# Kernel optimization log

Hardware: AMD Instinct MI355X
Metric: run time of the kernel (lower is better)

## Reference

```python
import jax, jax.numpy as jnp
import numpy as np

N_NODES = 50000


def gcn_conv(x, edge_index, W, b):
    """PyG GCNConv: add self-loops, sym-normalize, out = A_hat @ (x W) + b."""
    src, dst = edge_index[0], edge_index[1]
    n = x.shape[0]
    h = x @ W  # [N, out]
    # degree with self-loops (all edge weights = 1)
    deg = jax.ops.segment_sum(jnp.ones_like(dst, dtype=x.dtype), dst, num_segments=n) + 1.0
    dinv = jax.lax.rsqrt(deg)  # deg >= 1 so safe
    norm = dinv[src] * dinv[dst]  # [E]
    msgs = h[src] * norm[:, None]  # gather + scale
    agg = jax.ops.segment_sum(msgs, dst, num_segments=n)  # scatter-add
    agg = agg + h * (dinv * dinv)[:, None]  # self-loop term: norm_ii = dinv_i^2
    return agg + b


def setup_inputs() -> dict:
    key = jax.random.key(0)
    k_x, k_e, k_w1, k_w2 = jax.random.split(key, 4)
    in_ch, hid, out_ch = 256, 128, 128
    x = jax.random.normal(k_x, (N_NODES, in_ch), dtype=jnp.float32)
    edge_index = jax.random.randint(k_e, (2, 1_600_000), 0, N_NODES, dtype=jnp.int32)
    # Glorot-style init like PyG GCNConv
    W1 = jax.random.normal(k_w1, (in_ch, hid), dtype=jnp.float32) * (1.0 / np.sqrt(in_ch))
    b1 = jnp.zeros((hid,), dtype=jnp.float32)
    W2 = jax.random.normal(k_w2, (hid, out_ch), dtype=jnp.float32) * (1.0 / np.sqrt(hid))
    b2 = jnp.zeros((out_ch,), dtype=jnp.float32)
    return {"x": x, "edge_index": edge_index, "W1": W1, "b1": b1, "W2": W2, "b2": b2}


def reference(x, edge_index, W1, b1, W2, b2):
    # layer 1: GCNConv -> ReLU (dropout is identity in eval mode)
    h = jax.nn.relu(gcn_conv(x, edge_index, W1, b1))
    # layer 2: GCNConv -> ReLU
    out = jax.nn.relu(gcn_conv(h, edge_index, W2, b2))
    return out
```

## Files before the change

### kernel.cpp

```cpp
#include <hip/hip_runtime.h>
#include <cstdint>
#include <cstddef>


#define ELL_STRIDE 64
#define BCAP 8192
#define OVF_CAP 1024
#define PART_T 2048

typedef __attribute__((ext_vector_type(8))) short bf16x8;
typedef __attribute__((ext_vector_type(4))) float floatx4;

__device__ __forceinline__ unsigned short f2bf(float f) {
  unsigned int u = __float_as_uint(f);
  unsigned int r = (u + 0x7fffu + ((u >> 16) & 1u)) >> 16;
  return (unsigned short)r;
}
__device__ __forceinline__ float2 bfpair(unsigned int p) {
  float2 r;
  r.x = __uint_as_float(p << 16);
  r.y = __uint_as_float(p & 0xffff0000u);
  return r;
}

__global__ __launch_bounds__(256) void k_cvt_w(const float* __restrict__ W1,
                                               const float* __restrict__ W2,
                                               unsigned short* __restrict__ WT1,
                                               unsigned short* __restrict__ WT2,
                                               int* __restrict__ cursor,
                                               int* __restrict__ ovf_cnt,
                                               int NB) {
  int i = blockIdx.x * 256 + threadIdx.x;
  if (i < NB) cursor[i] = 0;
  if (i == NB) *ovf_cnt = 0;
  if (i < 128 * 256) {
    int n = i >> 8, k = i & 255;
    WT1[i] = f2bf(W1[k * 128 + n]);
  } else if (i < 128 * 256 + 128 * 128) {
    int j = i - 128 * 256;
    int n = j >> 7, k = j & 127;
    WT2[j] = f2bf(W2[k * 128 + n]);
  }
}

__global__ __launch_bounds__(256) void k_part(const int* __restrict__ src,
                                              const int* __restrict__ dst,
                                              int* __restrict__ cursor,
                                              unsigned int* __restrict__ part,
                                              int* __restrict__ ovf_cnt,
                                              int* __restrict__ ovf,
                                              int E, int NB) {
  __shared__ unsigned int stage1[PART_T];
  __shared__ unsigned int stage2[PART_T];
  __shared__ int hist[512];
  __shared__ int base_g[512];
  __shared__ int base_l[512];
  __shared__ int cl[512];
  __shared__ int sc[256];
  const int tid = threadIdx.x;
  const int e0 = blockIdx.x * PART_T;
  int valid = E - e0; if (valid > PART_T) valid = PART_T;

  hist[tid] = 0; hist[tid + 256] = 0;
  cl[tid] = 0; cl[tid + 256] = 0;
  __syncthreads();
  for (int i = tid; i < valid; i += 256) {
    int e = e0 + i;
    unsigned int v = (unsigned int)(src[e] & 0xffff) | ((unsigned int)dst[e] << 16);
    stage1[i] = v;
    atomicAdd(&hist[(v >> 16) >> 7], 1);
  }
  __syncthreads();
  for (int b = tid; b < NB; b += 256) base_g[b] = atomicAdd(&cursor[b], hist[b]);
  int h0 = hist[2 * tid], h1 = hist[2 * tid + 1];
  int pv = h0 + h1;
  sc[tid] = pv;
  __syncthreads();
  #pragma unroll
  for (int off = 1; off < 256; off <<= 1) {
    int t = (tid >= off) ? sc[tid - off] : 0;
    __syncthreads();
    sc[tid] += t;
    __syncthreads();
  }
  int excl = sc[tid] - pv;
  base_l[2 * tid] = excl;
  base_l[2 * tid + 1] = excl + h0;
  __syncthreads();
  for (int i = tid; i < valid; i += 256) {
    unsigned int v = stage1[i];
    int b = (v >> 16) >> 7;
    int pos = base_l[b] + atomicAdd(&cl[b], 1);
    stage2[pos] = v;
  }
  __syncthreads();
  for (int i = tid; i < valid; i += 256) {
    unsigned int v = stage2[i];
    int b = (v >> 16) >> 7;
    int g = base_g[b] + (i - base_l[b]);
    if (g < BCAP) {
      part[(size_t)b * BCAP + g] = v;
    } else {
      int p = atomicAdd(ovf_cnt, 1);
      if (p < OVF_CAP) { ovf[2 * p] = (int)(v & 0xffffu); ovf[2 * p + 1] = (int)(v >> 16); }
    }
  }
}

__global__ __launch_bounds__(256) void k_fill2(const unsigned int* __restrict__ part,
                                               const int* __restrict__ cursor,
                                               unsigned short* __restrict__ col,
                                               int* __restrict__ cnt,
                                               float* __restrict__ dinv,
                                               int* __restrict__ ovf_cnt,
                                               int* __restrict__ ovf, int N) {
  __shared__ unsigned short slab[128 * ELL_STRIDE];
  __shared__ int cl[128];
  const int tid = threadIdx.x;
  const int b = blockIdx.x;
  if (tid < 128) cl[tid] = 0;
  __syncthreads();
  int count = cursor[b]; if (count > BCAP) count = BCAP;
  const unsigned int* p = part + (size_t)b * BCAP;
  for (int i = tid; i < count; i += 256) {
    unsigned int v = p[i];
    int row = (v >> 16) & 127;
    int k = atomicAdd(&cl[row], 1);
    if (k < ELL_STRIDE) {
      slab[row * ELL_STRIDE + k] = (unsigned short)(v & 0xffffu);
    } else {
      int q = atomicAdd(ovf_cnt, 1);
      if (q < OVF_CAP) { ovf[2 * q] = (int)(v & 0xffffu); ovf[2 * q + 1] = (int)(v >> 16); }
    }
  }
  __syncthreads();
  uint4* d4 = (uint4*)(col + (size_t)b * 128 * ELL_STRIDE);
  const uint4* s4 = (const uint4*)slab;
  #pragma unroll
  for (int i = 0; i < (128 * ELL_STRIDE * 2) / (16 * 256); ++i)
    d4[i * 256 + tid] = s4[i * 256 + tid];
  if (tid < 128) {
    int node = b * 128 + tid;
    if (node < N) {
      int c = cl[tid];
      cnt[node] = c;
      dinv[node] = rsqrtf((float)c + 1.0f);
    }
  }
}

template <int K, bool AF32>
__global__ __launch_bounds__(256) void k_gemm_mfma(const void* __restrict__ Xv,
                                                   const unsigned short* __restrict__ WT,
                                                   const float* __restrict__ dinv,
                                                   unsigned short* __restrict__ hb,
                                                   int M) {
  constexpr int KP = K + 8;
  __shared__ unsigned short Bs[64 * KP];
  const int tid = threadIdx.x;
  const int wave = tid >> 6, lane = tid & 63;
  const int q = lane >> 4, m = lane & 15;
  const int row0 = blockIdx.x * 64 + wave * 16;
  const bool active = row0 < M;
  const int arow = row0 + m;

  floatx4 acc[8];
  #pragma unroll
  for (int nt = 0; nt < 8; ++nt) acc[nt] = (floatx4){0.f, 0.f, 0.f, 0.f};
  bf16x8 af[K / 32];

  #pragma unroll
  for (int half = 0; half < 2; ++half) {
    __syncthreads();
    for (int c = tid; c < 64 * (K / 8); c += 256) {
      int r = c / (K / 8), ko = (c % (K / 8)) * 8;
      *(uint4*)(Bs + r * KP + ko) =
          *(const uint4*)(WT + (size_t)(half * 64 + r) * K + ko);
    }
    __syncthreads();
    if (active) {
      #pragma unroll
      for (int ks = 0; ks < K / 32; ++ks) {
        const int k0 = ks * 32 + q * 8;
        if (half == 0) {
          if (AF32) {
            const float* X = (const float*)Xv;
            float4 a0 = *(const float4*)(X + (size_t)arow * K + k0);
            float4 a1 = *(const float4*)(X + (size_t)arow * K + k0 + 4);
            af[ks] = (bf16x8){(short)f2bf(a0.x), (short)f2bf(a0.y),
                              (short)f2bf(a0.z), (short)f2bf(a0.w),
                              (short)f2bf(a1.x), (short)f2bf(a1.y),
                              (short)f2bf(a1.z), (short)f2bf(a1.w)};
          } else {
            af[ks] = *(const bf16x8*)((const unsigned short*)Xv +
                                      (size_t)arow * K + k0);
          }
        }
        #pragma unroll
        for (int ntl = 0; ntl < 4; ++ntl) {
          bf16x8 bf = *(const bf16x8*)(Bs + (ntl * 16 + m) * KP + k0);
          acc[half * 4 + ntl] =
              __builtin_amdgcn_mfma_f32_16x16x32_bf16(af[ks], bf, acc[half * 4 + ntl],
                                                      0, 0, 0);
        }
      }
    }
  }
  if (!active) return;
  #pragma unroll
  for (int r = 0; r < 4; ++r) {
    int grow = row0 + q * 4 + r;
    float di = dinv[grow];
    #pragma unroll
    for (int nt = 0; nt < 8; ++nt)
      hb[(size_t)(nt >> 1) * M * 32 + (size_t)grow * 32 + (nt & 1) * 16 + m] =
          f2bf(acc[nt][r] * di);
  }
}

template <bool BF16OUT>
__global__ __launch_bounds__(256) void k_agg(const unsigned int* __restrict__ hb,
                                             const int* __restrict__ cnt,
                                             const unsigned short* __restrict__ col,
                                             const float* __restrict__ dinv,
                                             const int* __restrict__ ovf_cnt,
                                             const int* __restrict__ ovf,
                                             const float* __restrict__ bias,
                                             void* __restrict__ outv, int n) {
  const int tid = threadIdx.x;
  const int chunk = blockIdx.x & 3;
  const int nb = blockIdx.x >> 2;
  const int d = nb * 16 + (tid >> 4);
  const int u = tid & 15;
  if (d >= n) return;
  const unsigned int* slab = hb + (size_t)chunk * n * 16;

  float2 acc = bfpair(slab[(size_t)d * 16 + u]);

  int m = cnt[d]; if (m > ELL_STRIDE) m = ELL_STRIDE;
  const unsigned short* crow = col + (size_t)d * ELL_STRIDE;
  int k = 0;
  for (; k + 8 <= m; k += 8) {
    ushort4 ca = *(const ushort4*)(crow + k);
    ushort4 cb = *(const ushort4*)(crow + k + 4);
    unsigned int p0 = slab[(size_t)ca.x * 16 + u];
    unsigned int p1 = slab[(size_t)ca.y * 16 + u];
    unsigned int p2 = slab[(size_t)ca.z * 16 + u];
    unsigned int p3 = slab[(size_t)ca.w * 16 + u];
    unsigned int p4 = slab[(size_t)cb.x * 16 + u];
    unsigned int p5 = slab[(size_t)cb.y * 16 + u];
    unsigned int p6 = slab[(size_t)cb.z * 16 + u];
    unsigned int p7 = slab[(size_t)cb.w * 16 + u];
    float2 v0 = bfpair(p0), v1 = bfpair(p1), v2 = bfpair(p2), v3 = bfpair(p3);
    float2 v4 = bfpair(p4), v5 = bfpair(p5), v6 = bfpair(p6), v7 = bfpair(p7);
    acc.x += v0.x + v1.x + v2.x + v3.x + v4.x + v5.x + v6.x + v7.x;
    acc.y += v0.y + v1.y + v2.y + v3.y + v4.y + v5.y + v6.y + v7.y;
  }
  for (; k < m; ++k) {
    int c = crow[k];
    float2 v = bfpair(slab[(size_t)c * 16 + u]);
    acc.x += v.x; acc.y += v.y;
  }
  int V = *ovf_cnt; if (V > OVF_CAP) V = OVF_CAP;
  for (int j = 0; j < V; ++j) {
    if (ovf[2 * j + 1] == d) {
      float2 v = bfpair(slab[(size_t)ovf[2 * j] * 16 + u]);
      acc.x += v.x; acc.y += v.y;
    }
  }
  float di = dinv[d];
  float2 bv = *(const float2*)(bias + chunk * 32 + 2 * u);
  float rx = fmaxf(di * acc.x + bv.x, 0.f);
  float ry = fmaxf(di * acc.y + bv.y, 0.f);
  if (BF16OUT) {
    unsigned int pk = (unsigned int)f2bf(rx) | ((unsigned int)f2bf(ry) << 16);
    ((unsigned int*)outv)[(size_t)d * 64 + chunk * 16 + u] = pk;
  } else {
    *(float2*)((float*)outv + (size_t)d * 128 + chunk * 32 + 2 * u) =
        make_float2(rx, ry);
  }
}

extern "C" void kernel_launch(void* const* d_in, const int* in_sizes, int n_in,
                              void* d_out, int out_size, void* d_ws, size_t ws_size,
                              hipStream_t stream) {
  const float* x  = (const float*)d_in[0];
  const int*   ei = (const int*)d_in[1];
  const float* W1 = (const float*)d_in[2];
  const float* b1 = (const float*)d_in[3];
  const float* W2 = (const float*)d_in[4];
  const float* b2 = (const float*)d_in[5];
  float* out = (float*)d_out;

  const int IN_CH = 256;
  const int N = in_sizes[0] / IN_CH;
  const int E = in_sizes[1] / 2;
  const int NB = (N + 127) >> 7;

  const int* src = ei;
  const int* dst = ei + E;

  char* ws = (char*)d_ws;
  size_t off = 0;
  auto carve = [&](size_t bytes) {
    void* p = ws + off;
    off += (bytes + 255) & ~(size_t)255;
    return p;
  };
  int*            cursor  = (int*)carve((size_t)NB * 4);
  int*            ovf_cnt = (int*)carve(4);
  int*            ovf     = (int*)carve((size_t)OVF_CAP * 2 * 4);
  int*            cnt     = (int*)carve((size_t)N * 4);
  float*          dinv    = (float*)carve((size_t)N * 4);
  unsigned short* col     = (unsigned short*)carve((size_t)N * ELL_STRIDE * 2);
  unsigned short* hb      = (unsigned short*)carve((size_t)N * 128 * 2);
  unsigned short* WT1     = (unsigned short*)carve(128 * 256 * 2);
  unsigned short* WT2     = (unsigned short*)carve(128 * 128 * 2);
  char*           unionp  = (char*)carve((size_t)NB * BCAP * 4);
  unsigned int*   part    = (unsigned int*)unionp;
  unsigned short* aggbuf  = (unsigned short*)unionp;

  k_cvt_w<<<(128 * 256 + 128 * 128 + 255) / 256, 256, 0, stream>>>(
      W1, W2, WT1, WT2, cursor, ovf_cnt, NB);
  k_part <<<(E + PART_T - 1) / PART_T, 256, 0, stream>>>(src, dst, cursor, part,
                                                         ovf_cnt, ovf, E, NB);
  k_fill2<<<NB, 256, 0, stream>>>(part, cursor, col, cnt, dinv, ovf_cnt, ovf, N);

  int gblocks = (N + 63) / 64;
  int ablocks = 4 * ((N + 15) / 16);
  k_gemm_mfma<256, true ><<<gblocks, 256, 0, stream>>>(x, WT1, dinv, hb, N);
  k_agg<true ><<<ablocks, 256, 0, stream>>>((const unsigned int*)hb, cnt, col, dinv,
                                            ovf_cnt, ovf, b1, aggbuf, N);
  k_gemm_mfma<128, false><<<gblocks, 256, 0, stream>>>(aggbuf, WT2, dinv, hb, N);
  k_agg<false><<<ablocks, 256, 0, stream>>>((const unsigned int*)hb, cnt, col, dinv,
                                            ovf_cnt, ovf, b2, out, N);
}
```

Baseline: 266.5 us.

## Load full weight tile once in GEMM and widen aggregation gathers

The GEMM kernel now uses 512-thread blocks that stage the whole transposed weight matrix in shared memory once, instead of in two halves with extra barriers, and issues all 8 MFMA column tiles per k-step. The aggregation kernel stages each block's 32 ELL column lists in shared memory, gives each node 8 lanes that load 8-byte bf16 quads instead of 16 lanes loading 4-byte pairs, and unrolls the gather loop to 16 neighbours. The aim is fewer global index loads and more memory-level parallelism per thread. The cost is higher LDS use per GEMM block and more registers in the aggregation kernel, which could lower occupancy.

```diff
diff --git a/kernel.cpp b/kernel.cpp
--- a/kernel.cpp
+++ b/kernel.cpp
@@ -150,63 +150,59 @@
 }
 
 template <int K, bool AF32>
-__global__ __launch_bounds__(256) void k_gemm_mfma(const void* __restrict__ Xv,
+__global__ __launch_bounds__(512) void k_gemm_mfma(const void* __restrict__ Xv,
                                                    const unsigned short* __restrict__ WT,
                                                    const float* __restrict__ dinv,
                                                    unsigned short* __restrict__ hb,
                                                    int M) {
   constexpr int KP = K + 8;
-  __shared__ unsigned short Bs[64 * KP];
+  __shared__ unsigned short Bs[128 * KP];
   const int tid = threadIdx.x;
   const int wave = tid >> 6, lane = tid & 63;
   const int q = lane >> 4, m = lane & 15;
-  const int row0 = blockIdx.x * 64 + wave * 16;
+  const int row0 = blockIdx.x * 128 + wave * 16;
   const bool active = row0 < M;
   const int arow = row0 + m;
 
+  for (int c = tid; c < 128 * (K / 8); c += 512) {
+    int r = c / (K / 8), ko = (c % (K / 8)) * 8;
+    *(uint4*)(Bs + r * KP + ko) = *(const uint4*)(WT + (size_t)r * K + ko);
+  }
+
+  bf16x8 af[K / 32];
+  if (active) {
+    #pragma unroll
+    for (int ks = 0; ks < K / 32; ++ks) {
+      const int k0 = ks * 32 + q * 8;
+      if (AF32) {
+        const float* X = (const float*)Xv;
+        float4 a0 = *(const float4*)(X + (size_t)arow * K + k0);
+        float4 a1 = *(const float4*)(X + (size_t)arow * K + k0 + 4);
+        af[ks] = (bf16x8){(short)f2bf(a0.x), (short)f2bf(a0.y),
+                          (short)f2bf(a0.z), (short)f2bf(a0.w),
+                          (short)f2bf(a1.x), (short)f2bf(a1.y),
+                          (short)f2bf(a1.z), (short)f2bf(a1.w)};
+      } else {
+        af[ks] = *(const bf16x8*)((const unsigned short*)Xv +
+                                  (size_t)arow * K + k0);
+      }
+    }
+  }
+  __syncthreads();
+  if (!active) return;
+
   floatx4 acc[8];
   #pragma unroll
   for (int nt = 0; nt < 8; ++nt) acc[nt] = (floatx4){0.f, 0.f, 0.f, 0.f};
-  bf16x8 af[K / 32];
-
-  #pragma unroll
-  for (int half = 0; half < 2; ++half) {
-    __syncthreads();
-    for (int c = tid; c < 64 * (K / 8); c += 256) {
-      int r = c / (K / 8), ko = (c % (K / 8)) * 8;
-      *(uint4*)(Bs + r * KP + ko) =
-          *(const uint4*)(WT + (size_t)(half * 64 + r) * K + ko);
-    }
-    __syncthreads();
-    if (active) {
-      #pragma unroll
-      for (int ks = 0; ks < K / 32; ++ks) {
-        const int k0 = ks * 32 + q * 8;
-        if (half == 0) {
-          if (AF32) {
-            const float* X = (const float*)Xv;
-            float4 a0 = *(const float4*)(X + (size_t)arow * K + k0);
-            float4 a1 = *(const float4*)(X + (size_t)arow * K + k0 + 4);
-            af[ks] = (bf16x8){(short)f2bf(a0.x), (short)f2bf(a0.y),
-                              (short)f2bf(a0.z), (short)f2bf(a0.w),
-                              (short)f2bf(a1.x), (short)f2bf(a1.y),
-                              (short)f2bf(a1.z), (short)f2bf(a1.w)};
-          } else {
-            af[ks] = *(const bf16x8*)((const unsigned short*)Xv +
-                                      (size_t)arow * K + k0);
-          }
-        }
-        #pragma unroll
-        for (int ntl = 0; ntl < 4; ++ntl) {
-          bf16x8 bf = *(const bf16x8*)(Bs + (ntl * 16 + m) * KP + k0);
-          acc[half * 4 + ntl] =
-              __builtin_amdgcn_mfma_f32_16x16x32_bf16(af[ks], bf, acc[half * 4 + ntl],
-                                                      0, 0, 0);
-        }
-      }
-    }
-  }
-  if (!active) return;
+  #pragma unroll
+  for (int ks = 0; ks < K / 32; ++ks) {
+    const int k0 = ks * 32 + q * 8;
+    #pragma unroll
+    for (int nt = 0; nt < 8; ++nt) {
+      bf16x8 bf = *(const bf16x8*)(Bs + (nt * 16 + m) * KP + k0);
+      acc[nt] = __builtin_amdgcn_mfma_f32_16x16x32_bf16(af[ks], bf, acc[nt], 0, 0, 0);
+    }
+  }
   #pragma unroll
   for (int r = 0; r < 4; ++r) {
     int grow = row0 + q * 4 + r;
@@ -227,57 +223,103 @@
                                              const int* __restrict__ ovf,
                                              const float* __restrict__ bias,
                                              void* __restrict__ outv, int n) {
+  __shared__ unsigned short cols[32][ELL_STRIDE];
   const int tid = threadIdx.x;
   const int chunk = blockIdx.x & 3;
-  const int nb = blockIdx.x >> 2;
-  const int d = nb * 16 + (tid >> 4);
-  const int u = tid & 15;
+  const int nd0 = (blockIdx.x >> 2) * 32;
+  {
+    int s = tid * 16;
+    int node = nd0 + (s >> 6);
+    uint4 v0 = make_uint4(0, 0, 0, 0), v1 = v0;
+    if (node < n) {
+      v0 = *(const uint4*)(col + (size_t)node * ELL_STRIDE + (s & 63));
+      v1 = *(const uint4*)(col + (size_t)node * ELL_STRIDE + (s & 63) + 8);
+    }
+    *(uint4*)&cols[s >> 6][s & 63] = v0;
+    *(uint4*)&cols[s >> 6][(s & 63) + 8] = v1;
+  }
+  __syncthreads();
+  const int nodeL = tid >> 3;
+  const int d = nd0 + nodeL;
+  const int w = tid & 7;
   if (d >= n) return;
-  const unsigned int* slab = hb + (size_t)chunk * n * 16;
-
-  float2 acc = bfpair(slab[(size_t)d * 16 + u]);
+  const uint2* slab = (const uint2*)hb + (size_t)chunk * n * 8;
+  const unsigned short* lc = cols[nodeL];
+
+  uint2 sv = slab[(size_t)d * 8 + w];
+  float2 s0 = bfpair(sv.x), s1 = bfpair(sv.y);
+  float a0 = s0.x, a1 = s0.y, a2 = s1.x, a3 = s1.y;
 
   int m = cnt[d]; if (m > ELL_STRIDE) m = ELL_STRIDE;
-  const unsigned short* crow = col + (size_t)d * ELL_STRIDE;
   int k = 0;
+#define GATH(P)                                                   \
+  {                                                               \
+    float2 _x = bfpair((P).x), _y = bfpair((P).y);                \
+    a0 += _x.x; a1 += _x.y; a2 += _y.x; a3 += _y.y;               \
+  }
+  for (; k + 16 <= m; k += 16) {
+    ushort4 ca = *(const ushort4*)(lc + k);
+    ushort4 cb = *(const ushort4*)(lc + k + 4);
+    ushort4 cc = *(const ushort4*)(lc + k + 8);
+    ushort4 cd = *(const ushort4*)(lc + k + 12);
+    uint2 p0 = slab[(size_t)ca.x * 8 + w];
+    uint2 p1 = slab[(size_t)ca.y * 8 + w];
+    uint2 p2 = slab[(size_t)ca.z * 8 + w];
+    uint2 p3 = slab[(size_t)ca.w * 8 + w];
+    uint2 p4 = slab[(size_t)cb.x * 8 + w];
+    uint2 p5 = slab[(size_t)cb.y * 8 + w];
+    uint2 p6 = slab[(size_t)cb.z * 8 + w];
+    uint2 p7 = slab[(size_t)cb.w * 8 + w];
+    uint2 p8 = slab[(size_t)cc.x * 8 + w];
+    uint2 p9 = slab[(size_t)cc.y * 8 + w];
+    uint2 pa = slab[(size_t)cc.z * 8 + w];
+    uint2 pb = slab[(size_t)cc.w * 8 + w];
+    uint2 pc = slab[(size_t)cd.x * 8 + w];
+    uint2 pd = slab[(size_t)cd.y * 8 + w];
+    uint2 pe = slab[(size_t)cd.z * 8 + w];
+    uint2 pf = slab[(size_t)cd.w * 8 + w];
+    GATH(p0) GATH(p1) GATH(p2) GATH(p3) GATH(p4) GATH(p5) GATH(p6) GATH(p7)
+    GATH(p8) GATH(p9) GATH(pa) GATH(pb) GATH(pc) GATH(pd) GATH(pe) GATH(pf)
+  }
   for (; k + 8 <= m; k += 8) {
-    ushort4 ca = *(const ushort4*)(crow + k);
-    ushort4 cb = *(const ushort4*)(crow + k + 4);
-    unsigned int p0 = slab[(size_t)ca.x * 16 + u];
-    unsigned int p1 = slab[(size_t)ca.y * 16 + u];
-    unsigned int p2 = slab[(size_t)ca.z * 16 + u];
-    unsigned int p3 = slab[(size_t)ca.w * 16 + u];
-    unsigned int p4 = slab[(size_t)cb.x * 16 + u];
-    unsigned int p5 = slab[(size_t)cb.y * 16 + u];
-    unsigned int p6 = slab[(size_t)cb.z * 16 + u];
-    unsigned int p7 = slab[(size_t)cb.w * 16 + u];
-    float2 v0 = bfpair(p0), v1 = bfpair(p1), v2 = bfpair(p2), v3 = bfpair(p3);
-    float2 v4 = bfpair(p4), v5 = bfpair(p5), v6 = bfpair(p6), v7 = bfpair(p7);
-    acc.x += v0.x + v1.x + v2.x + v3.x + v4.x + v5.x + v6.x + v7.x;
-    acc.y += v0.y + v1.y + v2.y + v3.y + v4.y + v5.y + v6.y + v7.y;
+    ushort4 ca = *(const ushort4*)(lc + k);
+    ushort4 cb = *(const ushort4*)(lc + k + 4);
+    uint2 p0 = slab[(size_t)ca.x * 8 + w];
+    uint2 p1 = slab[(size_t)ca.y * 8 + w];
+    uint2 p2 = slab[(size_t)ca.z * 8 + w];
+    uint2 p3 = slab[(size_t)ca.w * 8 + w];
+    uint2 p4 = slab[(size_t)cb.x * 8 + w];
+    uint2 p5 = slab[(size_t)cb.y * 8 + w];
+    uint2 p6 = slab[(size_t)cb.z * 8 + w];
+    uint2 p7 = slab[(size_t)cb.w * 8 + w];
+    GATH(p0) GATH(p1) GATH(p2) GATH(p3) GATH(p4) GATH(p5) GATH(p6) GATH(p7)
   }
   for (; k < m; ++k) {
-    int c = crow[k];
-    float2 v = bfpair(slab[(size_t)c * 16 + u]);
-    acc.x += v.x; acc.y += v.y;
+    uint2 p = slab[(size_t)lc[k] * 8 + w];
+    GATH(p)
   }
   int V = *ovf_cnt; if (V > OVF_CAP) V = OVF_CAP;
   for (int j = 0; j < V; ++j) {
     if (ovf[2 * j + 1] == d) {
-      float2 v = bfpair(slab[(size_t)ovf[2 * j] * 16 + u]);
-      acc.x += v.x; acc.y += v.y;
-    }
-  }
+      uint2 p = slab[(size_t)ovf[2 * j] * 8 + w];
+      GATH(p)
+    }
+  }
+#undef GATH
   float di = dinv[d];
-  float2 bv = *(const float2*)(bias + chunk * 32 + 2 * u);
-  float rx = fmaxf(di * acc.x + bv.x, 0.f);
-  float ry = fmaxf(di * acc.y + bv.y, 0.f);
+  float4 bv = *(const float4*)(bias + chunk * 32 + w * 4);
+  float r0 = fmaxf(di * a0 + bv.x, 0.f);
+  float r1 = fmaxf(di * a1 + bv.y, 0.f);
+  float r2 = fmaxf(di * a2 + bv.z, 0.f);
+  float r3 = fmaxf(di * a3 + bv.w, 0.f);
   if (BF16OUT) {
-    unsigned int pk = (unsigned int)f2bf(rx) | ((unsigned int)f2bf(ry) << 16);
-    ((unsigned int*)outv)[(size_t)d * 64 + chunk * 16 + u] = pk;
+    uint2 pk;
+    pk.x = (unsigned int)f2bf(r0) | ((unsigned int)f2bf(r1) << 16);
+    pk.y = (unsigned int)f2bf(r2) | ((unsigned int)f2bf(r3) << 16);
+    ((uint2*)outv)[(size_t)d * 32 + chunk * 8 + w] = pk;
   } else {
-    *(float2*)((float*)outv + (size_t)d * 128 + chunk * 32 + 2 * u) =
-        make_float2(rx, ry);
+    *(float4*)((float*)outv + (size_t)d * 128 + chunk * 32 + w * 4) =
+        make_float4(r0, r1, r2, r3);
   }
 }
 
@@ -326,12 +368,12 @@
                                                          ovf_cnt, ovf, E, NB);
   k_fill2<<<NB, 256, 0, stream>>>(part, cursor, col, cnt, dinv, ovf_cnt, ovf, N);
 
-  int gblocks = (N + 63) / 64;
-  int ablocks = 4 * ((N + 15) / 16);
-  k_gemm_mfma<256, true ><<<gblocks, 256, 0, stream>>>(x, WT1, dinv, hb, N);
+  int gblocks = (N + 127) / 128;
+  int ablocks = 4 * ((N + 31) / 32);
+  k_gemm_mfma<256, true ><<<gblocks, 512, 0, stream>>>(x, WT1, dinv, hb, N);
   k_agg<true ><<<ablocks, 256, 0, stream>>>((const unsigned int*)hb, cnt, col, dinv,
                                             ovf_cnt, ovf, b1, aggbuf, N);
-  k_gemm_mfma<128, false><<<gblocks, 256, 0, stream>>>(aggbuf, WT2, dinv, hb, N);
+  k_gemm_mfma<128, false><<<gblocks, 512, 0, stream>>>(aggbuf, WT2, dinv, hb, N);
   k_agg<false><<<ablocks, 256, 0, stream>>>((const unsigned int*)hb, cnt, col, dinv,
                                             ovf_cnt, ovf, b2, out, N);
 }
```

New measurement: 253.1 us. 5.0% less time.
